# Kernel optimization log

Hardware: AMD Instinct MI355X
Metric: run time of the kernel (lower is better)

Reference implementation:

```python
import jax, jax.numpy as jnp
import numpy as np


def setup_inputs() -> dict:
    key = jax.random.key(0)
    k1, k2 = jax.random.split(key)
    queries = jax.random.normal(k1, (16, 1024, 256), dtype=jnp.float32)
    embedding = jax.random.normal(k2, (8192, 256), dtype=jnp.float32) * 0.02
    return {"queries": queries, "embedding": embedding}


def reference(queries, embedding):
    commitment_weight = 0.25
    # squared L2 distances: ||q||^2 + ||e||^2 - 2 q.e  -> [b, k, n]
    q_sq = jnp.sum(queries * queries, axis=-1, keepdims=True)          # [b,k,1]
    e_sq = jnp.sum(embedding * embedding, axis=-1)[None, None, :]      # [1,1,n]
    distances = q_sq + e_sq - 2.0 * jnp.einsum('bkc,nc->bkn', queries, embedding)
    code_indices = jnp.argmin(distances, axis=-1)                      # [b,k] int
    quantized = embedding[code_indices]                                # [b,k,c]
    commit_loss = jnp.mean((jax.lax.stop_gradient(queries) - quantized) ** 2)
    codebook_loss = jnp.mean((queries - jax.lax.stop_gradient(quantized)) ** 2)
    vq_loss = codebook_loss + commitment_weight * commit_loss
    # straight-through estimator
    quantized_st = queries + jax.lax.stop_gradient(quantized - queries)
    return (code_indices, quantized_st, vq_loss)
```

## Files before the change

kernel.cpp:

```cpp
#include <hip/hip_runtime.h>
#include <float.h>

typedef _Float16 half8 __attribute__((ext_vector_type(8)));
typedef _Float16 half4v __attribute__((ext_vector_type(4)));
typedef float f32x4 __attribute__((ext_vector_type(4)));

#define M_TOTAL 16384
#define N_CODES 8192
#define KDIM    256
#define BM 128
#define BN 128
#define BK 32
#define NK (KDIM / BK)
#define NB (N_CODES / BN)
#define TS 32
#define MARGIN 3.0e-3f
#define SQ_SCALE 512.0f
#define SE_SCALE 2048.0f
#define INV_PROD 1.9073486328125e-06f
#define RG 4
#define RCODES 1024
#define RNCH (N_CODES / RCODES)
#define RPB 1024
#define RM_BLOCKS 256
#define LR_BLOCKS 32

__global__ void prep_kernel(const float* __restrict__ src, _Float16* __restrict__ dst,
                            float* __restrict__ sq, float scale) {
    const int tid = threadIdx.x;
    const int row0 = blockIdx.x * 4;
    {
        const int r = row0 + (tid >> 6);
        const int e4 = tid & 63;
        const float4 v = *(const float4*)(src + (size_t)r * KDIM + e4 * 4);
        const half4v h = {(_Float16)(v.x * scale), (_Float16)(v.y * scale),
                          (_Float16)(v.z * scale), (_Float16)(v.w * scale)};
        ((half4v*)(dst + (size_t)r * KDIM))[e4] = h;
    }
    if (tid < 64) {
        const int grp = tid >> 4;
        const int sub = tid & 15;
        const int row = row0 + grp;
        const float* p = src + (size_t)row * KDIM + (sub >> 3) * 128 + (sub & 7);
        float r;
        {
            #pragma clang fp contract(off)
            float v = p[0];
            r = v * v;
            #pragma unroll
            for (int k = 1; k < 16; k++) { const float w = p[k * 8]; r = r + w * w; }
        }
        const float t1 = r  + __shfl_xor(r,  1, 64);
        const float t2 = t1 + __shfl_xor(t1, 2, 64);
        const float t3 = t2 + __shfl_xor(t2, 4, 64);
        const float t4 = t3 + __shfl_xor(t3, 8, 64);
        if (sub == 0) sq[row] = t4;
    }
}

__global__ void transpose_kernel(const float* __restrict__ E, float* __restrict__ ET) {
    __shared__ float tile[64][65];
    const int n0 = blockIdx.x * 64;
    const int k0 = blockIdx.y * 64;
    const int tid = threadIdx.x;
    const int r = tid >> 4;
    const int c4 = tid & 15;
    #pragma unroll
    for (int p = 0; p < 4; p++) {
        const int row = p * 16 + r;
        const float4 v = *(const float4*)(E + (size_t)(n0 + row) * KDIM + k0 + c4 * 4);
        tile[row][c4 * 4 + 0] = v.x;
        tile[row][c4 * 4 + 1] = v.y;
        tile[row][c4 * 4 + 2] = v.z;
        tile[row][c4 * 4 + 3] = v.w;
    }
    __syncthreads();
    #pragma unroll
    for (int p = 0; p < 4; p++) {
        const int d = p * 16 + r;
        float4 o;
        o.x = tile[c4 * 4 + 0][d];
        o.y = tile[c4 * 4 + 1][d];
        o.z = tile[c4 * 4 + 2][d];
        o.w = tile[c4 * 4 + 3][d];
        *(float4*)(ET + (size_t)(k0 + d) * N_CODES + n0 + c4 * 4) = o;
    }
}

union SMemU {
    _Float16 t[2][2][BM * TS];
    struct { unsigned k1[BM][2]; unsigned k2[BM][2]; } red;
};

__global__ __launch_bounds__(256, 2)
void mfma_top2_kernel(const _Float16* __restrict__ Qh, const _Float16* __restrict__ Eh,
                      const float* __restrict__ esq,
                      unsigned* __restrict__ k1s, unsigned* __restrict__ k2s) {
    __shared__ SMemU sm;
    const int tid = threadIdx.x;
    const int m0 = blockIdx.x * BM;
    const int n0 = blockIdx.y * BN;
    const int w = tid >> 6, lane = tid & 63;
    const int wm = w >> 1, wn = w & 1;
    const int qd = lane >> 4, c = lane & 15;
    const int which = w >> 1, half = w & 1;
    const _Float16* src = (which == 0) ? (Qh + (size_t)(m0 + half * 64) * KDIM)
                                       : (Eh + (size_t)(n0 + half * 64) * KDIM);
    const int hofs = half * 64 * TS;

    int srow[4], scol[4];
    #pragma unroll
    for (int it = 0; it < 4; it++) {
        const int u = it * 64 + lane;
        srow[it] = u >> 2;
        scol[it] = u & 3;
    }

    f32x4 acc[4][4];
    const f32x4 zero = {0.f, 0.f, 0.f, 0.f};
    #pragma unroll
    for (int mt = 0; mt < 4; mt++)
        #pragma unroll
        for (int nt = 0; nt < 4; nt++) acc[mt][nt] = zero;

    const int csw = (c >> 1) & 3;

    half8 pf[4];
    #pragma unroll
    for (int it = 0; it < 4; it++)
        pf[it] = *(const half8*)(src + (size_t)srow[it] * KDIM + scol[it] * 8);
    {
        _Float16* d0 = sm.t[0][which] + hofs;
        #pragma unroll
        for (int it = 0; it < 4; it++)
            *(half8*)(d0 + srow[it] * TS + (scol[it] ^ ((srow[it] >> 1) & 3)) * 8) = pf[it];
    }
    __syncthreads();

    for (int ki = 0; ki < NK; ki++) {
        if (ki + 1 < NK) {
            const int k0 = (ki + 1) * BK;
            #pragma unroll
            for (int it = 0; it < 4; it++)
                pf[it] = *(const half8*)(src + (size_t)srow[it] * KDIM + k0 + scol[it] * 8);
        }
        const _Float16* bq = sm.t[ki & 1][0];
        const _Float16* be = sm.t[ki & 1][1];
        half8 qa[4];
        #pragma unroll
        for (int mt = 0; mt < 4; mt++)
            qa[mt] = *(const half8*)(bq + (wm * 64 + mt * 16 + c) * TS + (qd ^ csw) * 8);
        #pragma unroll
        for (int nt = 0; nt < 4; nt++) {
            const half8 eh = *(const half8*)(be + (wn * 64 + nt * 16 + c) * TS + (qd ^ csw) * 8);
            #pragma unroll
            for (int mt = 0; mt < 4; mt++)
                acc[mt][nt] = __builtin_amdgcn_mfma_f32_16x16x32_f16(qa[mt], eh, acc[mt][nt], 0, 0, 0);
        }
        if (ki + 1 < NK) {
            _Float16* dn = sm.t[(ki + 1) & 1][which] + hofs;
            #pragma unroll
            for (int it = 0; it < 4; it++)
                *(half8*)(dn + srow[it] * TS + (scol[it] ^ ((srow[it] >> 1) & 3)) * 8) = pf[it];
            __syncthreads();
        }
    }

    float es8[4];
    #pragma unroll
    for (int nt = 0; nt < 4; nt++) es8[nt] = esq[n0 + wn * 64 + nt * 16 + c] + 8.0f;

    unsigned k1[16], k2[16];
    #pragma unroll
    for (int i = 0; i < 16; i++) { k1[i] = 0xFFFFFFFFu; k2[i] = 0xFFFFFFFFu; }

    #pragma unroll
    for (int mt = 0; mt < 4; mt++)
        #pragma unroll
        for (int nt = 0; nt < 4; nt++) {
            const unsigned nl = (unsigned)(wn * 64 + nt * 16 + c);
            #pragma unroll
            for (int r = 0; r < 4; r++) {
                const int i = mt * 4 + r;
                const float d = fmaf(acc[mt][nt][r], -INV_PROD, es8[nt]);
                const unsigned k = (__float_as_uint(d) & 0xFFFFFF80u) | nl;
                const unsigned t = min(k1[i], k);
                k2[i] = min(k2[i], max(k1[i], k));
                k1[i] = t;
            }
        }
    #pragma unroll
    for (int s = 1; s < 16; s <<= 1) {
        #pragma unroll
        for (int i = 0; i < 16; i++) {
            const unsigned ok1 = (unsigned)__shfl_xor((int)k1[i], s, 64);
            const unsigned ok2 = (unsigned)__shfl_xor((int)k2[i], s, 64);
            const unsigned t = min(k1[i], ok1);
            k2[i] = min(min(k2[i], ok2), max(k1[i], ok1));
            k1[i] = t;
        }
    }
    __syncthreads();
    if (c == 0) {
        #pragma unroll
        for (int mt = 0; mt < 4; mt++)
            #pragma unroll
            for (int r = 0; r < 4; r++) {
                const int ml = wm * 64 + mt * 16 + qd * 4 + r;
                sm.red.k1[ml][wn] = k1[mt * 4 + r];
                sm.red.k2[ml][wn] = k2[mt * 4 + r];
            }
    }
    __syncthreads();
    if (tid < BM) {
        const unsigned a1 = sm.red.k1[tid][0], b1 = sm.red.k1[tid][1];
        const unsigned a2 = sm.red.k2[tid][0], b2 = sm.red.k2[tid][1];
        const size_t o = (size_t)(m0 + tid) * NB + blockIdx.y;
        k1s[o] = min(a1, b1);
        k2s[o] = min(min(a2, b2), max(a1, b1));
    }
}

__global__ void finalize_kernel(const float* __restrict__ Q, const float* __restrict__ E,
                                const unsigned* __restrict__ k1s, const unsigned* __restrict__ k2s,
                                int* __restrict__ fcount, int* __restrict__ flist,
                                float* __restrict__ ws_loss, float* __restrict__ out) {
    const int q = blockIdx.x * 4 + (threadIdx.x >> 6);
    const int lane = threadIdx.x & 63;
    const unsigned k1 = k1s[(size_t)q * NB + lane];
    const unsigned k2 = k2s[(size_t)q * NB + lane];
    float v1 = __uint_as_float(k1 & 0xFFFFFF80u);
    int   gi = lane * 128 + (int)(k1 & 127u);
    float v2 = __uint_as_float(k2 & 0xFFFFFF80u);
    #pragma unroll
    for (int s = 1; s < 64; s <<= 1) {
        const float ov1 = __shfl_xor(v1, s, 64);
        const int   ogi = __shfl_xor(gi, s, 64);
        const float ov2 = __shfl_xor(v2, s, 64);
        const float nv2 = fminf(fminf(v2, ov2), fmaxf(v1, ov1));
        const bool take = (ov1 < v1) || (ov1 == v1 && ogi < gi);
        v1 = take ? ov1 : v1;
        gi = take ? ogi : gi;
        v2 = nv2;
    }
    if ((v2 - v1) < MARGIN) {
        if (lane == 0) flist[atomicAdd(fcount, 1)] = q;
        return;
    }

    if (lane == 0) out[q] = (float)gi;
    const float4 qv = *(const float4*)(Q + (size_t)q * KDIM + lane * 4);
    const float4 ev = *(const float4*)(E + (size_t)gi * KDIM + lane * 4);
    float4 st;
    {
        #pragma clang fp contract(off)
        st.x = qv.x + (ev.x - qv.x);
        st.y = qv.y + (ev.y - qv.y);
        st.z = qv.z + (ev.z - qv.z);
        st.w = qv.w + (ev.w - qv.w);
    }
    *(float4*)(out + M_TOTAL + (size_t)q * KDIM + lane * 4) = st;

    const float dx = qv.x - ev.x, dy = qv.y - ev.y, dz = qv.z - ev.z, dw = qv.w - ev.w;
    float s = dx * dx + dy * dy + dz * dz + dw * dw;
    #pragma unroll
    for (int off = 32; off > 0; off >>= 1) s += __shfl_down(s, off);
    if (lane == 0) ws_loss[q] = s;
}

__global__ __launch_bounds__(256, 4)
void refine_partial_kernel(const float* __restrict__ Q, const float* __restrict__ ET,
                           const float* __restrict__ qsq, const float* __restrict__ esq,
                           const int* __restrict__ fcount, const int* __restrict__ flist,
                           float* __restrict__ rp_v, int* __restrict__ rp_i) {
    const int cnt = *fcount;
    if (cnt == 0) return;
    const int ngroups = (cnt + RG - 1) / RG;
    const int ntasks = ngroups * RNCH;
    const int tid = threadIdx.x;
    const int w = tid >> 6, lane = tid & 63;
    __shared__ float qs[RG][KDIM];
    __shared__ float redv[4][RG];
    __shared__ int   redi[4][RG];

    for (int t = blockIdx.x; t < ntasks; t += RPB) {
        const int grp = t >> 3;
        const int chunk = t & (RNCH - 1);
        __syncthreads();
        {
            const int g = tid >> 6, c4 = tid & 63;
            const int fi = min(grp * RG + g, cnt - 1);
            const int q = flist[fi];
            *(float4*)&qs[g][c4 * 4] = *(const float4*)(Q + (size_t)q * KDIM + c4 * 4);
        }
        __syncthreads();

        const int nb = chunk * RCODES + tid * 4;
        float a[RG][4];
        #pragma unroll
        for (int g = 0; g < RG; g++)
            #pragma unroll
            for (int j = 0; j < 4; j++) a[g][j] = 0.f;

        for (int k4 = 0; k4 < KDIM / 4; k4++) {
            float4 qv[RG];
            #pragma unroll
            for (int g = 0; g < RG; g++) qv[g] = *(const float4*)&qs[g][k4 * 4];
            #pragma unroll
            for (int kk = 0; kk < 4; kk++) {
                const float4 ev = *(const float4*)(ET + (size_t)(k4 * 4 + kk) * N_CODES + nb);
                #pragma unroll
                for (int g = 0; g < RG; g++) {
                    const float qk = (kk == 0) ? qv[g].x : (kk == 1) ? qv[g].y
                                   : (kk == 2) ? qv[g].z : qv[g].w;
                    a[g][0] = fmaf(qk, ev.x, a[g][0]);
                    a[g][1] = fmaf(qk, ev.y, a[g][1]);
                    a[g][2] = fmaf(qk, ev.z, a[g][2]);
                    a[g][3] = fmaf(qk, ev.w, a[g][3]);
                }
            }
        }

        float es[4];
        #pragma unroll
        for (int j = 0; j < 4; j++) es[j] = esq[nb + j];

        #pragma unroll
        for (int g = 0; g < RG; g++) {
            const int fi = min(grp * RG + g, cnt - 1);
            const float qsv = qsq[flist[fi]];
            float bv = FLT_MAX; int bi = 0x7fffffff;
            #pragma unroll
            for (int j = 0; j < 4; j++) {
                float d;
                {
                    #pragma clang fp contract(off)
                    const float t1 = qsv + es[j];
                    d = t1 - 2.0f * a[g][j];
                }
                if (d < bv) { bv = d; bi = nb + j; }
            }
            #pragma unroll
            for (int s = 1; s < 64; s <<= 1) {
                const float ov = __shfl_xor(bv, s, 64);
                const int   oi = __shfl_xor(bi, s, 64);
                if (ov < bv || (ov == bv && oi < bi)) { bv = ov; bi = oi; }
            }
            if (lane == 0) { redv[w][g] = bv; redi[w][g] = bi; }
        }
        __syncthreads();
        if (tid < RG) {
            float fv = redv[0][tid]; int fidx = redi[0][tid];
            #pragma unroll
            for (int u = 1; u < 4; u++) {
                if (redv[u][tid] < fv || (redv[u][tid] == fv && redi[u][tid] < fidx)) {
                    fv = redv[u][tid]; fidx = redi[u][tid];
                }
            }
            rp_v[(size_t)t * RG + tid] = fv;
            rp_i[(size_t)t * RG + tid] = fidx;
        }
    }
}

__global__ void refine_merge_kernel(const float* __restrict__ Q, const float* __restrict__ E,
                                    const int* __restrict__ fcount, const int* __restrict__ flist,
                                    const float* __restrict__ rp_v, const int* __restrict__ rp_i,
                                    float* __restrict__ ws_loss, float* __restrict__ out) {
    const int cnt = *fcount;
    const int lane = threadIdx.x;
    for (int fi = blockIdx.x; fi < cnt; fi += RM_BLOCKS) {
        const int q = flist[fi];
        const int grp = fi >> 2, g = fi & 3;
        float bv = FLT_MAX; int bi = 0x7fffffff;
        if (lane < RNCH) {
            const size_t t = (size_t)(grp * RNCH + lane);
            bv = rp_v[t * RG + g];
            bi = rp_i[t * RG + g];
        }
        #pragma unroll
        for (int s = 1; s < 64; s <<= 1) {
            const float ov = __shfl_xor(bv, s, 64);
            const int   oi = __shfl_xor(bi, s, 64);
            if (ov < bv || (ov == bv && oi < bi)) { bv = ov; bi = oi; }
        }
        if (lane == 0) out[q] = (float)bi;

        const float4 qv = *(const float4*)(Q + (size_t)q * KDIM + lane * 4);
        const float4 ev = *(const float4*)(E + (size_t)bi * KDIM + lane * 4);
        float4 st;
        {
            #pragma clang fp contract(off)
            st.x = qv.x + (ev.x - qv.x);
            st.y = qv.y + (ev.y - qv.y);
            st.z = qv.z + (ev.z - qv.z);
            st.w = qv.w + (ev.w - qv.w);
        }
        *(float4*)(out + M_TOTAL + (size_t)q * KDIM + lane * 4) = st;
        const float dx = qv.x - ev.x, dy = qv.y - ev.y, dz = qv.z - ev.z, dw = qv.w - ev.w;
        float s = dx * dx + dy * dy + dz * dz + dw * dw;
        #pragma unroll
        for (int off = 32; off > 0; off >>= 1) s += __shfl_down(s, off);
        if (lane == 0) ws_loss[q] = s;
    }
}

__global__ void loss_reduce_kernel(const float* __restrict__ ws_loss, float* __restrict__ out) {
    const int tid = threadIdx.x;
    float s = 0.f;
    for (int i = blockIdx.x * 256 + tid; i < M_TOTAL; i += LR_BLOCKS * 256)
        s += ws_loss[i];
    #pragma unroll
    for (int off = 32; off > 0; off >>= 1) s += __shfl_down(s, off);
    __shared__ float ws[4];
    if ((tid & 63) == 0) ws[tid >> 6] = s;
    __syncthreads();
    if (tid == 0) {
        const float tot = (ws[0] + ws[1]) + (ws[2] + ws[3]);
        atomicAdd(out + M_TOTAL + (size_t)M_TOTAL * KDIM,
                  tot * (1.25f / (float)((size_t)M_TOTAL * KDIM)));
    }
}

extern "C" void kernel_launch(void* const* d_in, const int* in_sizes, int n_in,
                              void* d_out, int out_size, void* d_ws, size_t ws_size,
                              hipStream_t stream) {
    const float* Q = (const float*)d_in[0];
    const float* E = (const float*)d_in[1];
    float* out = (float*)d_out;

    char* ws = (char*)d_ws;
    _Float16* Qh  = (_Float16*)(ws);
    _Float16* Eh  = (_Float16*)(ws + (size_t)8  * 1024 * 1024);
    float* qsq    = (float*)   (ws + (size_t)12 * 1024 * 1024);
    float* esq    = qsq + M_TOTAL;
    unsigned* k1s = (unsigned*)(ws + (size_t)13 * 1024 * 1024);
    unsigned* k2s = (unsigned*)(ws + (size_t)17 * 1024 * 1024);
    int*   fcount = (int*)     (ws + (size_t)25 * 1024 * 1024);
    int*   flist  = fcount + 64;
    float* ws_loss= (float*)   (ws + (size_t)25 * 1024 * 1024 + 512 * 1024);
    float* ET     = (float*)   (ws + (size_t)26 * 1024 * 1024);
    float* rp_v   = (float*)k1s;
    int*   rp_i   = (int*)k2s;

    hipMemsetAsync(out + M_TOTAL + (size_t)M_TOTAL * KDIM, 0, sizeof(float), stream);
    hipMemsetAsync(fcount, 0, sizeof(int), stream);

    prep_kernel<<<M_TOTAL / 4, 256, 0, stream>>>(Q, Qh, qsq, SQ_SCALE);
    prep_kernel<<<N_CODES / 4, 256, 0, stream>>>(E, Eh, esq, SE_SCALE);
    transpose_kernel<<<dim3(N_CODES / 64, KDIM / 64), 256, 0, stream>>>(E, ET);

    mfma_top2_kernel<<<dim3(M_TOTAL / BM, N_CODES / BN), 256, 0, stream>>>(
        Qh, Eh, esq, k1s, k2s);

    finalize_kernel<<<M_TOTAL / 4, 256, 0, stream>>>(Q, E, k1s, k2s, fcount, flist, ws_loss, out);
    refine_partial_kernel<<<RPB, 256, 0, stream>>>(Q, ET, qsq, esq, fcount, flist, rp_v, rp_i);
    refine_merge_kernel<<<RM_BLOCKS, 64, 0, stream>>>(Q, E, fcount, flist, rp_v, rp_i, ws_loss, out);
    loss_reduce_kernel<<<LR_BLOCKS, 256, 0, stream>>>(ws_loss, out);
}
```

Baseline: 244.5 us.

## Load MFMA operands directly from global memory, dropping LDS staging

```diff
diff --git a/kernel.cpp b/kernel.cpp
--- a/kernel.cpp
+++ b/kernel.cpp
@@ -10,10 +10,7 @@
 #define KDIM    256
 #define BM 128
 #define BN 128
-#define BK 32
-#define NK (KDIM / BK)
 #define NB (N_CODES / BN)
-#define TS 32
 #define MARGIN 3.0e-3f
 #define SQ_SCALE 512.0f
 #define SE_SCALE 2048.0f
@@ -87,34 +84,20 @@
     }
 }
 
-union SMemU {
-    _Float16 t[2][2][BM * TS];
-    struct { unsigned k1[BM][2]; unsigned k2[BM][2]; } red;
-};
-
-__global__ __launch_bounds__(256, 2)
+__global__ __launch_bounds__(256, 4)
 void mfma_top2_kernel(const _Float16* __restrict__ Qh, const _Float16* __restrict__ Eh,
                       const float* __restrict__ esq,
                       unsigned* __restrict__ k1s, unsigned* __restrict__ k2s) {
-    __shared__ SMemU sm;
+    __shared__ struct { unsigned k1[BM][2]; unsigned k2[BM][2]; } red;
     const int tid = threadIdx.x;
-    const int m0 = blockIdx.x * BM;
-    const int n0 = blockIdx.y * BN;
+    const int n0 = blockIdx.x * BN;
+    const int m0 = blockIdx.y * BM;
     const int w = tid >> 6, lane = tid & 63;
     const int wm = w >> 1, wn = w & 1;
     const int qd = lane >> 4, c = lane & 15;
-    const int which = w >> 1, half = w & 1;
-    const _Float16* src = (which == 0) ? (Qh + (size_t)(m0 + half * 64) * KDIM)
-                                       : (Eh + (size_t)(n0 + half * 64) * KDIM);
-    const int hofs = half * 64 * TS;
-
-    int srow[4], scol[4];
-    #pragma unroll
-    for (int it = 0; it < 4; it++) {
-        const int u = it * 64 + lane;
-        srow[it] = u >> 2;
-        scol[it] = u & 3;
-    }
+
+    const _Float16* qb = Qh + (size_t)(m0 + wm * 64 + c) * KDIM + qd * 8;
+    const _Float16* eb = Eh + (size_t)(n0 + wn * 64 + c) * KDIM + qd * 8;
 
     f32x4 acc[4][4];
     const f32x4 zero = {0.f, 0.f, 0.f, 0.f};
@@ -123,47 +106,21 @@
         #pragma unroll
         for (int nt = 0; nt < 4; nt++) acc[mt][nt] = zero;
 
-    const int csw = (c >> 1) & 3;
-
-    half8 pf[4];
-    #pragma unroll
-    for (int it = 0; it < 4; it++)
-        pf[it] = *(const half8*)(src + (size_t)srow[it] * KDIM + scol[it] * 8);
-    {
-        _Float16* d0 = sm.t[0][which] + hofs;
-        #pragma unroll
-        for (int it = 0; it < 4; it++)
-            *(half8*)(d0 + srow[it] * TS + (scol[it] ^ ((srow[it] >> 1) & 3)) * 8) = pf[it];
-    }
-    __syncthreads();
-
-    for (int ki = 0; ki < NK; ki++) {
-        if (ki + 1 < NK) {
-            const int k0 = (ki + 1) * BK;
-            #pragma unroll
-            for (int it = 0; it < 4; it++)
-                pf[it] = *(const half8*)(src + (size_t)srow[it] * KDIM + k0 + scol[it] * 8);
-        }
-        const _Float16* bq = sm.t[ki & 1][0];
-        const _Float16* be = sm.t[ki & 1][1];
-        half8 qa[4];
+    #pragma unroll
+    for (int ki = 0; ki < 8; ki++) {
+        const int k0 = ki * 32;
+        half8 qa[4], ef[4];
         #pragma unroll
         for (int mt = 0; mt < 4; mt++)
-            qa[mt] = *(const half8*)(bq + (wm * 64 + mt * 16 + c) * TS + (qd ^ csw) * 8);
-        #pragma unroll
-        for (int nt = 0; nt < 4; nt++) {
-            const half8 eh = *(const half8*)(be + (wn * 64 + nt * 16 + c) * TS + (qd ^ csw) * 8);
+            qa[mt] = *(const half8*)(qb + (size_t)mt * 16 * KDIM + k0);
+        #pragma unroll
+        for (int nt = 0; nt < 4; nt++)
+            ef[nt] = *(const half8*)(eb + (size_t)nt * 16 * KDIM + k0);
+        #pragma unroll
+        for (int nt = 0; nt < 4; nt++)
             #pragma unroll
             for (int mt = 0; mt < 4; mt++)
-                acc[mt][nt] = __builtin_amdgcn_mfma_f32_16x16x32_f16(qa[mt], eh, acc[mt][nt], 0, 0, 0);
-        }
-        if (ki + 1 < NK) {
-            _Float16* dn = sm.t[(ki + 1) & 1][which] + hofs;
-            #pragma unroll
-            for (int it = 0; it < 4; it++)
-                *(half8*)(dn + srow[it] * TS + (scol[it] ^ ((srow[it] >> 1) & 3)) * 8) = pf[it];
-            __syncthreads();
-        }
+                acc[mt][nt] = __builtin_amdgcn_mfma_f32_16x16x32_f16(qa[mt], ef[nt], acc[mt][nt], 0, 0, 0);
     }
 
     float es8[4];
@@ -200,22 +157,21 @@
             k1[i] = t;
         }
     }
-    __syncthreads();
     if (c == 0) {
         #pragma unroll
         for (int mt = 0; mt < 4; mt++)
             #pragma unroll
             for (int r = 0; r < 4; r++) {
                 const int ml = wm * 64 + mt * 16 + qd * 4 + r;
-                sm.red.k1[ml][wn] = k1[mt * 4 + r];
-                sm.red.k2[ml][wn] = k2[mt * 4 + r];
+                red.k1[ml][wn] = k1[mt * 4 + r];
+                red.k2[ml][wn] = k2[mt * 4 + r];
             }
     }
     __syncthreads();
     if (tid < BM) {
-        const unsigned a1 = sm.red.k1[tid][0], b1 = sm.red.k1[tid][1];
-        const unsigned a2 = sm.red.k2[tid][0], b2 = sm.red.k2[tid][1];
-        const size_t o = (size_t)(m0 + tid) * NB + blockIdx.y;
+        const unsigned a1 = red.k1[tid][0], b1 = red.k1[tid][1];
+        const unsigned a2 = red.k2[tid][0], b2 = red.k2[tid][1];
+        const size_t o = (size_t)(m0 + tid) * NB + blockIdx.x;
         k1s[o] = min(a1, b1);
         k2s[o] = min(min(a2, b2), max(a1, b1));
     }
@@ -450,7 +406,7 @@
     prep_kernel<<<N_CODES / 4, 256, 0, stream>>>(E, Eh, esq, SE_SCALE);
     transpose_kernel<<<dim3(N_CODES / 64, KDIM / 64), 256, 0, stream>>>(E, ET);
 
-    mfma_top2_kernel<<<dim3(M_TOTAL / BM, N_CODES / BN), 256, 0, stream>>>(
+    mfma_top2_kernel<<<dim3(N_CODES / BN, M_TOTAL / BM), 256, 0, stream>>>(
         Qh, Eh, esq, k1s, k2s);
 
     finalize_kernel<<<M_TOTAL / 4, 256, 0, stream>>>(Q, E, k1s, k2s, fcount, flist, ws_loss, out);
```

Measured after the change: 375.3 us. 53.5% more time.
